# Kernel optimization log

Hardware: AMD Instinct MI355X
Metric: run time of the kernel (lower is better)

The kernel has to match this reference:

```python
import jax, jax.numpy as jnp
import numpy as np

N = 100000
E = 1600000
F_IN = 128
H = 128


def setup_inputs() -> dict:
    key = jax.random.key(0)
    ks = jax.random.split(key, 12)
    x = jax.random.normal(ks[0], (N, F_IN), dtype=jnp.float32)
    edge_index = jax.random.randint(ks[1], (2, E), 0, N, dtype=jnp.int64)
    s = 1.0 / np.sqrt(F_IN)
    sh = 1.0 / np.sqrt(H)
    inp = {"x": x, "edge_index": edge_index}
    # SAGEConv params: lin_l (neighbor agg, with bias), lin_r (root, no bias)
    inp["W1l"] = jax.random.uniform(ks[2], (H, F_IN), jnp.float32, -s, s)
    inp["b1"] = jnp.zeros((H,), jnp.float32)
    inp["W1r"] = jax.random.uniform(ks[3], (H, F_IN), jnp.float32, -s, s)
    inp["W2l"] = jax.random.uniform(ks[4], (H, H), jnp.float32, -sh, sh)
    inp["b2"] = jnp.zeros((H,), jnp.float32)
    inp["W2r"] = jax.random.uniform(ks[5], (H, H), jnp.float32, -sh, sh)
    inp["W3l"] = jax.random.uniform(ks[6], (H, H), jnp.float32, -sh, sh)
    inp["b3"] = jnp.zeros((H,), jnp.float32)
    inp["W3r"] = jax.random.uniform(ks[7], (H, H), jnp.float32, -sh, sh)
    inp["Wo"] = jax.random.uniform(ks[8], (1, H), jnp.float32, -sh, sh)
    inp["bo"] = jnp.zeros((1,), jnp.float32)
    return inp


def _sage_max(h, src, dst, Wl, bl, Wr):
    # max-aggregate source features at destination nodes (empty -> 0, as PyG)
    m = jax.ops.segment_max(h[src], dst, num_segments=N)  # [N, d]
    m = jnp.where(jnp.isfinite(m), m, jnp.zeros_like(m))
    return m @ Wl.T + bl + h @ Wr.T


def reference(x, edge_index, W1l, b1, W1r, W2l, b2, W2r, W3l, b3, W3r, Wo, bo):
    src, dst = edge_index[0], edge_index[1]
    h1 = jax.nn.elu(_sage_max(x, src, dst, W1l, b1, W1r))
    h2 = jax.nn.elu(_sage_max(h1, src, dst, W2l, b2, W2r)) + h1
    h3 = jax.nn.elu(_sage_max(h2, src, dst, W3l, b3, W3r)) + h2
    return jax.nn.sigmoid(h3 @ Wo.T + bo)  # [N, 1]
```

## Files before the change

kernel.cpp:

```cpp
#include <hip/hip_runtime.h>
#include <hip/hip_fp16.h>
#include <math.h>

#define HDIM 128

#define BSHIFT 7
#define BW 128
#define BCAP 4096
#define NBKMAX 1024
#define CHUNK 4096

typedef __attribute__((ext_vector_type(8))) _Float16 f16x8;
typedef __attribute__((ext_vector_type(2))) _Float16 f16x2;
typedef __attribute__((ext_vector_type(16))) float f32x16;
typedef unsigned int uint32;
typedef unsigned short u16;

__device__ __forceinline__ uint32 hmax2u(uint32 a, uint32 b) {
    f16x2 ha = __builtin_bit_cast(f16x2, a);
    f16x2 hb = __builtin_bit_cast(f16x2, b);
    f16x2 r = __builtin_elementwise_max(ha, hb);
    return __builtin_bit_cast(uint32, r);
}
__device__ __forceinline__ uint32 hadd2u(uint32 a, uint32 b) {
    f16x2 ha = __builtin_bit_cast(f16x2, a);
    f16x2 hb = __builtin_bit_cast(f16x2, b);
    f16x2 r = ha + hb;
    return __builtin_bit_cast(uint32, r);
}


__global__ __launch_bounds__(256) void bucket_bin(
    const int* __restrict__ ei, int E_, int nbk,
    int* __restrict__ bucketCnt, uint32* __restrict__ tmp)
{
    __shared__ int cnt[NBKMAX];
    __shared__ int gbase[NBKMAX];
    const int t = threadIdx.x;
    const int start = blockIdx.x * CHUNK;
    const int end = min(start + CHUNK, E_);

    for (int i = t; i < nbk; i += 256) cnt[i] = 0;
    __syncthreads();
    for (int e = start + t; e < end; e += 256)
        atomicAdd(&cnt[ei[E_ + e] >> BSHIFT], 1);
    __syncthreads();
    for (int i = t; i < nbk; i += 256) {
        int c = cnt[i];
        gbase[i] = c ? atomicAdd(&bucketCnt[i], c) : 0;
    }
    __syncthreads();
    for (int i = t; i < nbk; i += 256) cnt[i] = 0;
    __syncthreads();
    for (int e = start + t; e < end; e += 256) {
        int d = ei[E_ + e];
        int s = ei[e];
        int b = d >> BSHIFT;
        int r = atomicAdd(&cnt[b], 1);
        tmp[(size_t)b * BCAP + gbase[b] + r] =
            ((uint32)(d & (BW - 1)) << 17) | (uint32)s;
    }
}

__global__ __launch_bounds__(1024) void bucket_scan(
    const int* __restrict__ bucketCnt, int* __restrict__ bucketBase,
    int nbk, int* __restrict__ off, int N_, int E_) {
    __shared__ int sd[1024];
    int t = threadIdx.x;
    int v = (t < nbk) ? bucketCnt[t] : 0;
    sd[t] = v;
    __syncthreads();
    for (int ofs = 1; ofs < 1024; ofs <<= 1) {
        int add = (t >= ofs) ? sd[t - ofs] : 0;
        __syncthreads();
        sd[t] += add;
        __syncthreads();
    }
    if (t < nbk) bucketBase[t] = sd[t] - v;
    if (t == 0) off[N_] = E_;
}

__global__ __launch_bounds__(256) void bucket_csr(
    const uint32* __restrict__ tmp, const int* __restrict__ bucketCnt,
    const int* __restrict__ bucketBase,
    int* __restrict__ off, int* __restrict__ srcs, int N_)
{
    __shared__ int lc[BW];
    __shared__ int lo[BW];
    __shared__ int sd[256];
    const int b = blockIdx.x, t = threadIdx.x;
    const int cnt = bucketCnt[b], base = bucketBase[b];
    const uint32* tp = tmp + (size_t)b * BCAP;

    if (t < BW) lc[t] = 0;
    __syncthreads();
    for (int i = t; i < cnt; i += 256) atomicAdd(&lc[tp[i] >> 17], 1);
    __syncthreads();

    int v = (t < BW) ? lc[t] : 0;
    sd[t] = v;
    __syncthreads();
    for (int ofs = 1; ofs < 256; ofs <<= 1) {
        int add = (t >= ofs) ? sd[t - ofs] : 0;
        __syncthreads();
        sd[t] += add;
        __syncthreads();
    }
    if (t < BW) lo[t] = sd[t] - v;
    __syncthreads();

    for (int i = t; i < BW; i += 256) {
        int node = b * BW + i;
        if (node < N_) off[node] = base + lo[i];
    }
    if (t < BW) lc[t] = lo[t];
    __syncthreads();
    for (int i = t; i < cnt; i += 256) {
        uint32 p = tp[i];
        int dl = p >> 17, s = p & 0x1FFFF;
        int pos = base + atomicAdd(&lc[dl], 1);
        srcs[pos] = s;
    }
}


__global__ void cast_x(const float* __restrict__ x, uint32* __restrict__ xb, int n2) {
    int i = blockIdx.x * 256 + threadIdx.x;
    if (i >= n2) return;
    float2 v = ((const float2*)x)[i];
    f16x2 h = { (_Float16)v.x, (_Float16)v.y };
    xb[i] = __builtin_bit_cast(uint32, h);
}

__global__ void cast_weights_packed(
    const float* __restrict__ W1l, const float* __restrict__ W1r,
    const float* __restrict__ W2l, const float* __restrict__ W2r,
    const float* __restrict__ W3l, const float* __restrict__ W3r,
    f16x8* __restrict__ PW)
{
    int tid = blockIdx.x * 256 + threadIdx.x;
    if (tid >= 3 * 4096) return;
    int layer = tid >> 12, rem = tid & 4095;
    int g = rem >> 10, ks = (rem >> 6) & 15, lane = rem & 63;
    int col = g * 32 + (lane & 31), kq = lane >> 5;
    const float* src;
    if (layer == 0)      src = (ks < 8) ? W1l : W1r;
    else if (layer == 1) src = (ks < 8) ? W2l : W2r;
    else                 src = (ks < 8) ? W3l : W3r;
    int kk = (ks & 7) * 16 + kq * 8;
    f16x8 v;
#pragma unroll
    for (int j = 0; j < 8; ++j) v[j] = (_Float16)src[col * HDIM + kk + j];
    PW[tid] = v;
}


#define ESTRIDE 136
#define EDGE_CAP 832

#define RED16(m0,m1,m2,m3,V) do { \
    m0 = hmax2u(m0, (V)[0].x); m1 = hmax2u(m1, (V)[0].y); \
    m2 = hmax2u(m2, (V)[0].z); m3 = hmax2u(m3, (V)[0].w); \
    m0 = hmax2u(m0, (V)[1].x); m1 = hmax2u(m1, (V)[1].y); \
    m2 = hmax2u(m2, (V)[1].z); m3 = hmax2u(m3, (V)[1].w); \
    m0 = hmax2u(m0, (V)[2].x); m1 = hmax2u(m1, (V)[2].y); \
    m2 = hmax2u(m2, (V)[2].z); m3 = hmax2u(m3, (V)[2].w); \
    m0 = hmax2u(m0, (V)[3].x); m1 = hmax2u(m1, (V)[3].y); \
    m2 = hmax2u(m2, (V)[3].z); m3 = hmax2u(m3, (V)[3].w); \
} while (0)

template<bool L>
__device__ __forceinline__ void issue_batch(
    const uint4* __restrict__ hp, const int* __restrict__ srcs,
    const int* sedge, int estart, int eb, int e1, int es, int ch, uint4* v)
{
    int last = e1 - 1;
#pragma unroll
    for (int k = 0; k < 4; ++k) {
        int idx = min(eb + es + 4 * k, last);
        int s = L ? sedge[idx - estart] : srcs[idx];
        v[k] = hp[(size_t)s * 16 + ch];
    }
}

template<bool L>
__device__ __forceinline__ void gather8(
    const uint4* __restrict__ hp, const int* __restrict__ srcs,
    const int* sedge, int estart, int offv, int es, int ch, int w,
    uint4* sm)
{
    const uint32 NINF = 0xFC00FC00u;
    uint4 vb[2][4];

    int e0 = __shfl(offv, 0), e1 = __shfl(offv, 1);
    bool has = e1 > e0;
    if (has) issue_batch<L>(hp, srcs, sedge, estart, e0, e1, es, ch, vb[0]);

#pragma unroll
    for (int i = 0; i < 8; ++i) {
        int e0n = 0, e1n = 0; bool hasn = false;
        if (i + 1 < 8) {
            e0n = __shfl(offv, i + 1); e1n = __shfl(offv, i + 2);
            hasn = e1n > e0n;
            if (hasn) issue_batch<L>(hp, srcs, sedge, estart, e0n, e1n, es, ch, vb[(i + 1) & 1]);
        }
        uint32 m0 = NINF, m1 = NINF, m2 = NINF, m3 = NINF;
        if (has) {
            RED16(m0, m1, m2, m3, vb[i & 1]);
            for (int eb = e0 + 16; eb < e1; eb += 16) {
                issue_batch<L>(hp, srcs, sedge, estart, eb, e1, es, ch, vb[i & 1]);
                RED16(m0, m1, m2, m3, vb[i & 1]);
            }
        }
        m0 = hmax2u(m0, __shfl_xor(m0, 16)); m0 = hmax2u(m0, __shfl_xor(m0, 32));
        m1 = hmax2u(m1, __shfl_xor(m1, 16)); m1 = hmax2u(m1, __shfl_xor(m1, 32));
        m2 = hmax2u(m2, __shfl_xor(m2, 16)); m2 = hmax2u(m2, __shfl_xor(m2, 32));
        m3 = hmax2u(m3, __shfl_xor(m3, 16)); m3 = hmax2u(m3, __shfl_xor(m3, 32));
        if (es == 0) {
            int row = w * 8 + i;
            uint4 rr = make_uint4(0u, 0u, 0u, 0u);
            if (has) { rr.x = m0; rr.y = m1; rr.z = m2; rr.w = m3; }
            sm[row * 16 + (ch ^ (row & 7))] = rr;
        }
        e0 = e0n; e1 = e1n; has = hasn;
    }
}

__global__ __launch_bounds__(256, 8) void fused_layer(
    const uint32* __restrict__ hb,
    const int* __restrict__ off, const int* __restrict__ srcs,
    uint4* __restrict__ outb,
    const uint4* __restrict__ PW,
    const float* __restrict__ bias,
    int use_res,
    const float* __restrict__ Wo, const float* __restrict__ bo,
    float* __restrict__ out, int n_nodes)
{
    __shared__ alignas(16) char smemA[32 * ESTRIDE * 2];
    __shared__ uint4 sh[512];
    __shared__ int soff[33];
    __shared__ int sedge[EDGE_CAP];
    uint4*     sm = (uint4*)smemA;
    _Float16*  ho = (_Float16*)smemA;

    const int t = threadIdx.x, lane = t & 63, w = t >> 6;
    const int base = blockIdx.x * 32;
    const int l31 = lane & 31, kq = lane >> 5;
    const uint4* hp = (const uint4*)hb;

    if (t < 33) soff[t] = off[min(base + t, n_nodes)];

#pragma unroll
    for (int r = 0; r < 2; ++r) {
        int g = r * 256 + t;
        int row = g >> 4, c = g & 15;
        sh[row * 16 + (c ^ (row & 7))] = hp[(size_t)(base + row) * 16 + c];
    }

    const int estart = off[base];
    const int eend = off[min(base + 32, n_nodes)];
    const int ecnt = eend - estart;
    const bool useLds = (ecnt <= EDGE_CAP);
    const int scount = useLds ? ecnt : 0;
    for (int i = t; i < scount; i += 256) sedge[i] = srcs[estart + i];
    __syncthreads();

    const int es = lane >> 4, ch = lane & 15;
    const int offv = soff[w * 8 + min(lane, 8)];
    if (useLds) gather8<true >(hp, srcs, sedge, estart, offv, es, ch, w, sm);
    else        gather8<false>(hp, srcs, sedge, estart, offv, es, ch, w, sm);
    __syncthreads();

    f32x16 acc = {};
#pragma unroll
    for (int k = 0; k < 8; ++k) {
        f16x8 a = __builtin_bit_cast(f16x8, sm[l31 * 16 + ((2 * k + kq) ^ (l31 & 7))]);
        f16x8 b = __builtin_bit_cast(f16x8, PW[(w * 16 + k) * 64 + lane]);
        acc = __builtin_amdgcn_mfma_f32_32x32x16_f16(a, b, acc, 0, 0, 0);
    }
#pragma unroll
    for (int k = 0; k < 8; ++k) {
        f16x8 a = __builtin_bit_cast(f16x8, sh[l31 * 16 + ((2 * k + kq) ^ (l31 & 7))]);
        f16x8 b = __builtin_bit_cast(f16x8, PW[(w * 16 + 8 + k) * 64 + lane]);
        acc = __builtin_amdgcn_mfma_f32_32x32x16_f16(a, b, acc, 0, 0, 0);
    }

    __syncthreads();

    const int C = w * 32 + l31;
    const float bv = bias[C];
#pragma unroll
    for (int r = 0; r < 16; ++r) {
        int row = (r & 3) + 8 * (r >> 2) + 4 * kq;
        float v = acc[r] + bv;
        v = (v > 0.f) ? v : (__expf(v) - 1.f);
        ho[row * ESTRIDE + C] = (_Float16)v;
    }
    __syncthreads();

#pragma unroll
    for (int r = 0; r < 2; ++r) {
        int g = r * 256 + t;
        int row = g >> 4, c = g & 15;
        int R = base + row;
        bool valid = (R < n_nodes);
        uint4 v = *(const uint4*)&ho[row * ESTRIDE + c * 8];
        if (use_res) {
            uint4 rv = sh[row * 16 + (c ^ (row & 7))];
            v.x = hadd2u(v.x, rv.x); v.y = hadd2u(v.y, rv.y);
            v.z = hadd2u(v.z, rv.z); v.w = hadd2u(v.w, rv.w);
        }
        if (outb) {
            if (valid) outb[(size_t)R * 16 + c] = v;
        } else {
            const float* wo = Wo + c * 8;
            f16x2 a0 = __builtin_bit_cast(f16x2, v.x);
            f16x2 a1 = __builtin_bit_cast(f16x2, v.y);
            f16x2 a2 = __builtin_bit_cast(f16x2, v.z);
            f16x2 a3 = __builtin_bit_cast(f16x2, v.w);
            float s = (float)a0.x * wo[0] + (float)a0.y * wo[1]
                    + (float)a1.x * wo[2] + (float)a1.y * wo[3]
                    + (float)a2.x * wo[4] + (float)a2.y * wo[5]
                    + (float)a3.x * wo[6] + (float)a3.y * wo[7];
#pragma unroll
            for (int o = 8; o; o >>= 1) s += __shfl_down(s, o, 16);
            if (valid && (t & 15) == 0)
                out[R] = 1.f / (1.f + expf(-(s + bo[0])));
        }
    }
}


extern "C" void kernel_launch(void* const* d_in, const int* in_sizes, int n_in,
                              void* d_out, int out_size, void* d_ws, size_t ws_size,
                              hipStream_t stream) {
    const float* x   = (const float*)d_in[0];
    const int*   ei  = (const int*)d_in[1];
    const float* W1l = (const float*)d_in[2];
    const float* b1  = (const float*)d_in[3];
    const float* W1r = (const float*)d_in[4];
    const float* W2l = (const float*)d_in[5];
    const float* b2  = (const float*)d_in[6];
    const float* W2r = (const float*)d_in[7];
    const float* W3l = (const float*)d_in[8];
    const float* b3  = (const float*)d_in[9];
    const float* W3r = (const float*)d_in[10];
    const float* Wo  = (const float*)d_in[11];
    const float* bo  = (const float*)d_in[12];
    float* out = (float*)d_out;

    const int N_ = in_sizes[0] / HDIM;
    const int E_ = in_sizes[1] / 2;
    const int Np = (N_ + 127) & ~127;
    const int nbk = (N_ + BW - 1) / BW;

    size_t o = 0;
    auto carve = [&](size_t bytes) { size_t r = o; o = (o + bytes + 255) & ~255ULL; return r; };
    char* ws = (char*)d_ws;
    int* off        = (int*)(ws + carve((size_t)(N_ + 1) * 4));
    int* bucketCnt  = (int*)(ws + carve((size_t)NBKMAX * 4));
    int* bucketBase = (int*)(ws + carve((size_t)NBKMAX * 4));
    int* srcs       = (int*)(ws + carve((size_t)E_ * 4));
    uint32* tmp     = (uint32*)(ws + carve((size_t)nbk * BCAP * 4));
    uint4* PW       = (uint4*)(ws + carve((size_t)3 * 4096 * 16));
    uint32* XB      = (uint32*)(ws + carve((size_t)Np * 64 * 4));
    uint32* H1B     = (uint32*)(ws + carve((size_t)Np * 64 * 4));
    (void)ws_size; (void)n_in; (void)out_size;

    (void)hipMemsetAsync(bucketCnt, 0, (size_t)NBKMAX * 4, stream);
    bucket_bin<<<(E_ + CHUNK - 1) / CHUNK, 256, 0, stream>>>(ei, E_, nbk, bucketCnt, tmp);
    bucket_scan<<<1, 1024, 0, stream>>>(bucketCnt, bucketBase, nbk, off, N_, E_);
    bucket_csr<<<nbk, 256, 0, stream>>>(tmp, bucketCnt, bucketBase, off, srcs, N_);

    cast_weights_packed<<<(3 * 4096 + 255) / 256, 256, 0, stream>>>(
        W1l, W1r, W2l, W2r, W3l, W3r, (f16x8*)PW);
    cast_x<<<(N_ * 64 + 255) / 256, 256, 0, stream>>>(x, XB, N_ * 64);

    const int nbF = (N_ + 31) / 32;

    const uint4* PW1 = PW;
    const uint4* PW2 = PW + 4096;
    const uint4* PW3 = PW + 8192;

    fused_layer<<<nbF, 256, 0, stream>>>(XB, off, srcs, (uint4*)H1B, PW1, b1,
                                         0, nullptr, nullptr, nullptr, N_);
    fused_layer<<<nbF, 256, 0, stream>>>(H1B, off, srcs, (uint4*)XB, PW2, b2,
                                         1, nullptr, nullptr, nullptr, N_);
    fused_layer<<<nbF, 256, 0, stream>>>(XB, off, srcs, nullptr, PW3, b3,
                                         1, Wo, bo, out, N_);
}
```

Baseline: 368.3 us.

## Merge prep kernels, stage CSR bucket in LDS, lower fused_layer occupancy hint

Merges edge binning, weight packing and the x cast into one heterogeneous launch, removing two kernel launches and letting the independent work run concurrently. bucket_csr now loads its bucket into shared memory and builds the sorted source list there, then writes it out contiguously instead of scattering to global memory. The fused_layer launch-bounds occupancy hint drops from 8 to 6 blocks per CU, giving the compiler more registers per thread at the cost of fewer resident waves. bucket_csr now holds about 32KB of extra static shared memory, which reduces how many of its blocks fit on a CU.

```diff
diff --git a/kernel.cpp b/kernel.cpp
--- a/kernel.cpp
+++ b/kernel.cpp
@@ -30,37 +30,66 @@
 }
 
 
-__global__ __launch_bounds__(256) void bucket_bin(
-    const int* __restrict__ ei, int E_, int nbk,
-    int* __restrict__ bucketCnt, uint32* __restrict__ tmp)
+__global__ __launch_bounds__(256) void prep(
+    const float* __restrict__ x, const int* __restrict__ ei,
+    const float* __restrict__ W1l, const float* __restrict__ W1r,
+    const float* __restrict__ W2l, const float* __restrict__ W2r,
+    const float* __restrict__ W3l, const float* __restrict__ W3r,
+    f16x8* __restrict__ PW, uint32* __restrict__ xb,
+    int* __restrict__ bucketCnt, uint32* __restrict__ tmp,
+    int E_, int N_, int nbk, int nbB, int nbW)
 {
     __shared__ int cnt[NBKMAX];
     __shared__ int gbase[NBKMAX];
-    const int t = threadIdx.x;
-    const int start = blockIdx.x * CHUNK;
-    const int end = min(start + CHUNK, E_);
-
-    for (int i = t; i < nbk; i += 256) cnt[i] = 0;
-    __syncthreads();
-    for (int e = start + t; e < end; e += 256)
-        atomicAdd(&cnt[ei[E_ + e] >> BSHIFT], 1);
-    __syncthreads();
-    for (int i = t; i < nbk; i += 256) {
-        int c = cnt[i];
-        gbase[i] = c ? atomicAdd(&bucketCnt[i], c) : 0;
-    }
-    __syncthreads();
-    for (int i = t; i < nbk; i += 256) cnt[i] = 0;
-    __syncthreads();
-    for (int e = start + t; e < end; e += 256) {
-        int d = ei[E_ + e];
-        int s = ei[e];
-        int b = d >> BSHIFT;
-        int r = atomicAdd(&cnt[b], 1);
-        tmp[(size_t)b * BCAP + gbase[b] + r] =
-            ((uint32)(d & (BW - 1)) << 17) | (uint32)s;
-    }
-}
+    const int bid = blockIdx.x, t = threadIdx.x;
+
+    if (bid < nbB) {
+        const int start = bid * CHUNK;
+        const int end = min(start + CHUNK, E_);
+        for (int i = t; i < nbk; i += 256) cnt[i] = 0;
+        __syncthreads();
+        for (int e = start + t; e < end; e += 256)
+            atomicAdd(&cnt[ei[E_ + e] >> BSHIFT], 1);
+        __syncthreads();
+        for (int i = t; i < nbk; i += 256) {
+            int c = cnt[i];
+            gbase[i] = c ? atomicAdd(&bucketCnt[i], c) : 0;
+        }
+        __syncthreads();
+        for (int i = t; i < nbk; i += 256) cnt[i] = 0;
+        __syncthreads();
+        for (int e = start + t; e < end; e += 256) {
+            int d = ei[E_ + e];
+            int s = ei[e];
+            int b = d >> BSHIFT;
+            int r = atomicAdd(&cnt[b], 1);
+            tmp[(size_t)b * BCAP + gbase[b] + r] =
+                ((uint32)(d & (BW - 1)) << 17) | (uint32)s;
+        }
+    } else if (bid < nbB + nbW) {
+        int tid = (bid - nbB) * 256 + t;
+        if (tid >= 3 * 4096) return;
+        int layer = tid >> 12, rem = tid & 4095;
+        int g = rem >> 10, ks = (rem >> 6) & 15, lane = rem & 63;
+        int col = g * 32 + (lane & 31), kq = lane >> 5;
+        const float* src;
+        if (layer == 0)      src = (ks < 8) ? W1l : W1r;
+        else if (layer == 1) src = (ks < 8) ? W2l : W2r;
+        else                 src = (ks < 8) ? W3l : W3r;
+        int kk = (ks & 7) * 16 + kq * 8;
+        f16x8 v;
+#pragma unroll
+        for (int j = 0; j < 8; ++j) v[j] = (_Float16)src[col * HDIM + kk + j];
+        PW[tid] = v;
+    } else {
+        int i = (bid - nbB - nbW) * 256 + t;
+        if (i >= N_ * 64) return;
+        float2 v = ((const float2*)x)[i];
+        f16x2 h = { (_Float16)v.x, (_Float16)v.y };
+        xb[i] = __builtin_bit_cast(uint32, h);
+    }
+}
+
 
 __global__ __launch_bounds__(1024) void bucket_scan(
     const int* __restrict__ bucketCnt, int* __restrict__ bucketBase,
@@ -80,11 +109,14 @@
     if (t == 0) off[N_] = E_;
 }
 
+
 __global__ __launch_bounds__(256) void bucket_csr(
     const uint32* __restrict__ tmp, const int* __restrict__ bucketCnt,
     const int* __restrict__ bucketBase,
     int* __restrict__ off, int* __restrict__ srcs, int N_)
 {
+    __shared__ uint32 stmp[BCAP];
+    __shared__ int sout[BCAP];
     __shared__ int lc[BW];
     __shared__ int lo[BW];
     __shared__ int sd[256];
@@ -92,9 +124,11 @@
     const int cnt = bucketCnt[b], base = bucketBase[b];
     const uint32* tp = tmp + (size_t)b * BCAP;
 
+    for (int i = t; i < cnt; i += 256) stmp[i] = tp[i];
     if (t < BW) lc[t] = 0;
     __syncthreads();
-    for (int i = t; i < cnt; i += 256) atomicAdd(&lc[tp[i] >> 17], 1);
+
+    for (int i = t; i < cnt; i += 256) atomicAdd(&lc[stmp[i] >> 17], 1);
     __syncthreads();
 
     int v = (t < BW) ? lc[t] : 0;
@@ -115,43 +149,14 @@
     }
     if (t < BW) lc[t] = lo[t];
     __syncthreads();
+
     for (int i = t; i < cnt; i += 256) {
-        uint32 p = tp[i];
-        int dl = p >> 17, s = p & 0x1FFFF;
-        int pos = base + atomicAdd(&lc[dl], 1);
-        srcs[pos] = s;
-    }
-}
-
-
-__global__ void cast_x(const float* __restrict__ x, uint32* __restrict__ xb, int n2) {
-    int i = blockIdx.x * 256 + threadIdx.x;
-    if (i >= n2) return;
-    float2 v = ((const float2*)x)[i];
-    f16x2 h = { (_Float16)v.x, (_Float16)v.y };
-    xb[i] = __builtin_bit_cast(uint32, h);
-}
-
-__global__ void cast_weights_packed(
-    const float* __restrict__ W1l, const float* __restrict__ W1r,
-    const float* __restrict__ W2l, const float* __restrict__ W2r,
-    const float* __restrict__ W3l, const float* __restrict__ W3r,
-    f16x8* __restrict__ PW)
-{
-    int tid = blockIdx.x * 256 + threadIdx.x;
-    if (tid >= 3 * 4096) return;
-    int layer = tid >> 12, rem = tid & 4095;
-    int g = rem >> 10, ks = (rem >> 6) & 15, lane = rem & 63;
-    int col = g * 32 + (lane & 31), kq = lane >> 5;
-    const float* src;
-    if (layer == 0)      src = (ks < 8) ? W1l : W1r;
-    else if (layer == 1) src = (ks < 8) ? W2l : W2r;
-    else                 src = (ks < 8) ? W3l : W3r;
-    int kk = (ks & 7) * 16 + kq * 8;
-    f16x8 v;
-#pragma unroll
-    for (int j = 0; j < 8; ++j) v[j] = (_Float16)src[col * HDIM + kk + j];
-    PW[tid] = v;
+        uint32 p = stmp[i];
+        int pos = atomicAdd(&lc[p >> 17], 1);
+        sout[pos] = (int)(p & 0x1FFFF);
+    }
+    __syncthreads();
+    for (int i = t; i < cnt; i += 256) srcs[base + i] = sout[i];
 }
 
 
@@ -226,7 +231,7 @@
     }
 }
 
-__global__ __launch_bounds__(256, 8) void fused_layer(
+__global__ __launch_bounds__(256, 6) void fused_layer(
     const uint32* __restrict__ hb,
     const int* __restrict__ off, const int* __restrict__ srcs,
     uint4* __restrict__ outb,
@@ -368,13 +373,17 @@
     (void)ws_size; (void)n_in; (void)out_size;
 
     (void)hipMemsetAsync(bucketCnt, 0, (size_t)NBKMAX * 4, stream);
-    bucket_bin<<<(E_ + CHUNK - 1) / CHUNK, 256, 0, stream>>>(ei, E_, nbk, bucketCnt, tmp);
+
+    const int nbB = (E_ + CHUNK - 1) / CHUNK;
+    const int nbW = (3 * 4096 + 255) / 256;
+    const int nbX = (N_ * 64 + 255) / 256;
+    prep<<<nbB + nbW + nbX, 256, 0, stream>>>(
+        x, ei, W1l, W1r, W2l, W2r, W3l, W3r,
+        (f16x8*)PW, XB, bucketCnt, tmp, E_, N_, nbk, nbB, nbW);
+
     bucket_scan<<<1, 1024, 0, stream>>>(bucketCnt, bucketBase, nbk, off, N_, E_);
+
     bucket_csr<<<nbk, 256, 0, stream>>>(tmp, bucketCnt, bucketBase, off, srcs, N_);
-
-    cast_weights_packed<<<(3 * 4096 + 255) / 256, 256, 0, stream>>>(
-        W1l, W1r, W2l, W2r, W3l, W3r, (f16x8*)PW);
-    cast_x<<<(N_ * 64 + 255) / 256, 256, 0, stream>>>(x, XB, N_ * 64);
 
     const int nbF = (N_ + 31) / 32;
 
```

Result: faster. 347.8 us (-5.6%).
